# Performance work log

Hardware: AMD Instinct MI355X
Metric: run time of the kernel (lower is better)

The kernel has to match this reference:

```python
import jax, jax.numpy as jnp
import numpy as np

B_, N_, D_ = 8, 1024, 64
H_, DH_ = 4, 16
DI_, DS_, DTR_ = 128, 64, 4
MAXP = 512


def _ln(x, w, b, eps=1e-5):
    m = jnp.mean(x, -1, keepdims=True)
    v = jnp.mean((x - m) ** 2, -1, keepdims=True)
    return (x - m) * jax.lax.rsqrt(v + eps) * w + b


def _attn(x, drop_mask, Wq, Wkv, Wo, bo, rel_emb):
    b, n, d = x.shape
    scale = DH_ ** -0.5
    q = (x @ Wq).reshape(b, n, H_, DH_).transpose(0, 2, 1, 3)
    kv = x @ Wkv
    k = kv[..., :d].reshape(b, n, H_, DH_).transpose(0, 2, 1, 3)
    v = kv[..., d:].reshape(b, n, H_, DH_).transpose(0, 2, 1, 3)
    dots = jnp.einsum('bhid,bhjd->bhij', q, k) * scale
    seq = jnp.arange(n)
    dist = jnp.clip(seq[:, None] - seq[None, :], -MAXP, MAXP) + MAXP
    rpe = rel_emb[dist]  # (n, n, DH_)
    dots = dots + jnp.einsum('bhid,ijd->bhij', q, rpe) * scale
    # stochastic key drop: Bernoulli(0.3) positions get -1e12
    dots = dots + drop_mask.astype(dots.dtype) * (-1e12)
    attn = jax.nn.softmax(dots, axis=-1)
    out = jnp.einsum('bhij,bhjd->bhid', attn, v)
    out = out.transpose(0, 2, 1, 3).reshape(b, n, H_ * DH_)
    return out @ Wo + bo


def _mamba(x, W_in, conv_w, conv_b, W_xproj, W_dt, b_dt, A_log, Dm, W_out):
    b, n, _ = x.shape
    xz = x @ W_in                      # (b, n, 2*DI_)
    u, z = xz[..., :DI_], xz[..., DI_:]
    uc = u.transpose(0, 2, 1)          # (b, DI_, n)
    uc = jax.lax.conv_general_dilated(
        uc, conv_w[:, None, :], (1,), ((3, 0),),
        feature_group_count=DI_, dimension_numbers=('NCH', 'OIH', 'NCH'))
    uc = uc + conv_b[None, :, None]
    u = jax.nn.silu(uc).transpose(0, 2, 1)  # (b, n, DI_)
    xdb = u @ W_xproj                  # (b, n, DTR_+2*DS_)
    dt = jax.nn.softplus(xdb[..., :DTR_] @ W_dt + b_dt)  # (b, n, DI_)
    Bm = xdb[..., DTR_:DTR_ + DS_]
    Cm = xdb[..., DTR_ + DS_:]
    A = -jnp.exp(A_log)                # (DI_, DS_)

    def step(h, inp):
        dt_t, B_t, C_t, u_t = inp      # (b,DI_),(b,DS_),(b,DS_),(b,DI_)
        dA = jnp.exp(dt_t[..., None] * A)
        h = h * dA + (dt_t * u_t)[..., None] * B_t[:, None, :]
        y = jnp.einsum('bds,bs->bd', h, C_t)
        return h, y

    h0 = jnp.zeros((b, DI_, DS_), x.dtype)
    xs = (dt.transpose(1, 0, 2), Bm.transpose(1, 0, 2),
          Cm.transpose(1, 0, 2), u.transpose(1, 0, 2))
    _, ys = jax.lax.scan(step, h0, xs)
    y = ys.transpose(1, 0, 2) + u * Dm
    y = y * jax.nn.silu(z)
    return y @ W_out


def _rmsgn(x, gamma, eps=1e-5, groups=4):
    shp = x.shape
    dpg = shp[-1] // groups
    xg = x.reshape(shp[:-1] + (groups, dpg))
    rms = jnp.sqrt(jnp.sum(xg * xg, -1, keepdims=True)) * (dpg ** -0.5)
    return (xg / (rms + eps)).reshape(shp) * gamma


def _ff1(x, c1_w, c1_b, d1_w, d1_b):
    # SwiGLUConvDeconv1d(64, 256, kernel=4, shift=1); x: (b, s2, 64)
    s2 = x.shape[1]
    xc = x.transpose(0, 2, 1)
    xc = jnp.pad(xc, ((0, 0), (0, 0), (3, 3)))
    xc = jax.lax.conv_general_dilated(
        xc, c1_w, (1,), 'VALID', dimension_numbers=('NCH', 'OIH', 'NCH'))
    xc = xc + c1_b[None, :, None]
    gate = jax.nn.silu(xc[:, 256:, :])
    xc = xc[:, :256, :] * gate
    # ConvTranspose1d stride 1 == conv with flipped kernel, full padding
    w = jnp.flip(d1_w, -1).transpose(1, 0, 2)  # (64, 256, 4)
    xc = jax.lax.conv_general_dilated(
        xc, w, (1,), ((3, 3),), dimension_numbers=('NCH', 'OIH', 'NCH'))
    xc = xc + d1_b[None, :, None]
    out = xc.transpose(0, 2, 1)
    return out[:, 3:3 + s2, :]


def _forward(x, drop_mask, ln1_w, ln1_b, Wq, Wkv, Wo, bo, rel_emb,
             ln2_w, ln2_b, W_in, conv_w, conv_b, W_xproj, W_dt, b_dt,
             A_log, Dm, W_out, gamma, c1_w, c1_b, d1_w, d1_b, ln3_w, ln3_b):
    xt = _ln(x, ln1_w, ln1_b)
    xt = _attn(xt, drop_mask, Wq, Wkv, Wo, bo, rel_emb) + x
    x = x + xt  # dropout p=0 -> identity (faithful to original residual math)
    xt = _ln(x, ln2_w, ln2_b)
    m = _mamba(xt, W_in, conv_w, conv_b, W_xproj, W_dt, b_dt, A_log, Dm, W_out)
    m = jnp.where(m >= 0, m, 0.01 * m)  # leaky_relu
    m = _rmsgn(m, gamma)
    m = m + 0.5 * _ff1(m, c1_w, c1_b, d1_w, d1_b)
    x = x + m
    return _ln(x, ln3_w, ln3_b)


def setup_inputs() -> dict:
    ks = jax.random.split(jax.random.key(0), 16)
    g = lambda i, shp, s: jax.random.normal(ks[i], shp, dtype=jnp.float32) * s
    A_log = jnp.log(jnp.tile(jnp.arange(1, DS_ + 1, dtype=jnp.float32)[None, :], (DI_, 1)))
    return {
        'x': jax.random.normal(ks[0], (B_, N_, D_), dtype=jnp.float32),
        'drop_mask': jax.random.bernoulli(ks[1], 0.3, (B_, H_, N_, N_)),
        'ln1_w': jnp.ones((D_,), jnp.float32), 'ln1_b': jnp.zeros((D_,), jnp.float32),
        'Wq': g(2, (D_, D_), 0.1), 'Wkv': g(3, (D_, 2 * D_), 0.1),
        'Wo': g(4, (D_, D_), 0.1), 'bo': jnp.zeros((D_,), jnp.float32),
        'rel_emb': g(5, (2 * MAXP + 1, DH_), 0.02),
        'ln2_w': jnp.ones((D_,), jnp.float32), 'ln2_b': jnp.zeros((D_,), jnp.float32),
        'W_in': g(6, (D_, 2 * DI_), 0.1),
        'conv_w': g(7, (DI_, 4), 0.2), 'conv_b': jnp.zeros((DI_,), jnp.float32),
        'W_xproj': g(8, (DI_, DTR_ + 2 * DS_), 0.1),
        'W_dt': g(9, (DTR_, DI_), 0.1), 'b_dt': jnp.zeros((DI_,), jnp.float32),
        'A_log': A_log, 'Dm': jnp.ones((DI_,), jnp.float32),
        'W_out': g(10, (DI_, D_), 0.1),
        'gamma': jnp.ones((D_,), jnp.float32),
        'c1_w': g(11, (512, 64, 4), 0.1), 'c1_b': jnp.zeros((512,), jnp.float32),
        'd1_w': g(12, (256, 64, 4), 0.1), 'd1_b': jnp.zeros((64,), jnp.float32),
        'ln3_w': jnp.ones((D_,), jnp.float32), 'ln3_b': jnp.zeros((D_,), jnp.float32),
    }


def reference(x, drop_mask, ln1_w, ln1_b, Wq, Wkv, Wo, bo, rel_emb,
              ln2_w, ln2_b, W_in, conv_w, conv_b, W_xproj, W_dt, b_dt,
              A_log, Dm, W_out, gamma, c1_w, c1_b, d1_w, d1_b, ln3_w, ln3_b):
    return _forward(x, drop_mask, ln1_w, ln1_b, Wq, Wkv, Wo, bo, rel_emb,
                    ln2_w, ln2_b, W_in, conv_w, conv_b, W_xproj, W_dt, b_dt,
                    A_log, Dm, W_out, gamma, c1_w, c1_b, d1_w, d1_b, ln3_w, ln3_b)
```

## Files before the change

kernel.cpp:

```cpp
#include <hip/hip_runtime.h>
#include <math.h>


__device__ __forceinline__ float wsum64(float v){
#pragma unroll
  for(int m=32;m>0;m>>=1) v += __shfl_xor(v, m, 64);
  return v;
}
__device__ __forceinline__ float wmax64(float v){
#pragma unroll
  for(int m=32;m>0;m>>=1) v = fmaxf(v, __shfl_xor(v, m, 64));
  return v;
}
__device__ __forceinline__ float silu_f(float x){ return x / (1.f + __expf(-x)); }

__global__ __launch_bounds__(256) void k_ln1_qkv(
    const float* __restrict__ x, const float* __restrict__ w1, const float* __restrict__ b1,
    const float* __restrict__ Wq, const float* __restrict__ Wkv,
    const float* __restrict__ rel, const float* __restrict__ c1w,
    float* __restrict__ qb, float2* __restrict__ kvT,
    float* __restrict__ relT, float* __restrict__ c1wT){
  int lane = threadIdx.x & 63, warp = threadIdx.x >> 6;
  int token = blockIdx.x*4 + warp;
  __shared__ float xt[4][64];
  float xv = x[(size_t)token*64 + lane];
  float mean = wsum64(xv) * 0.015625f;
  float dlt = xv - mean;
  float var = wsum64(dlt*dlt) * 0.015625f;
  float xn = dlt * rsqrtf(var + 1e-5f) * w1[lane] + b1[lane];
  xt[warp][lane] = xn;
  __syncthreads();
  float aq=0.f, ak=0.f, av=0.f;
#pragma unroll 4
  for(int dd=0; dd<64; ++dd){
    float xd = xt[warp][dd];
    aq += xd * Wq[dd*64 + lane];
    ak += xd * Wkv[dd*128 + lane];
    av += xd * Wkv[dd*128 + 64 + lane];
  }
  int b = token >> 10, i = token & 1023;
  int h = lane >> 4, dh = lane & 15;
  size_t o  = (((size_t)(b*4 + h))*1024 + i)*16 + dh;
  size_t oT = (((size_t)(b*4 + h))*16 + dh)*1024 + i;
  qb[o]=aq;
  kvT[oT] = make_float2(ak, av);

  if (blockIdx.x < 65){
    int idx = blockIdx.x*256 + threadIdx.x;
    if (idx < 16*1025){
      int c = idx / 1025;
      int d = idx - c*1025;
      relT[idx] = rel[d*16 + c];
    }
  } else if (blockIdx.x < 577){
    int idx = (blockIdx.x-65)*256 + threadIdx.x;
    int row = idx >> 9;
    int ii  = idx & 511;
    c1wT[idx] = c1w[(size_t)ii*256 + row];
  }
}

__global__ __launch_bounds__(256) void k_kmax(
    const float2* __restrict__ kvT, float* __restrict__ Kmax){
  int bh = blockIdx.x; int tid = threadIdx.x;
  const float2* base = kvT + (size_t)bh*16*1024;
  float mx = 0.f;
#pragma unroll
  for(int r=0;r<4;++r){
    int j = tid + 256*r;
    float ss = 0.f;
#pragma unroll
    for(int c=0;c<16;++c){ float2 kv = base[c*1024 + j]; ss += kv.x*kv.x; }
    mx = fmaxf(mx, ss);
  }
  mx = wmax64(mx);
  __shared__ float red[4];
  int lane = tid&63, wv = tid>>6;
  if(lane==0) red[wv]=mx;
  __syncthreads();
  if(tid==0) Kmax[bh] = sqrtf(fmaxf(fmaxf(red[0],red[1]),fmaxf(red[2],red[3])));
}

__global__ __launch_bounds__(256, 3) void k_attn(
    const float* __restrict__ qb, const float2* __restrict__ kvT,
    const int* __restrict__ dmask, const float* __restrict__ relT,
    const float* __restrict__ Kmax, float* __restrict__ attn_raw){
  int tid = threadIdx.x;
  int lane = tid & 63, wv = tid >> 6;
  int bh  = blockIdx.y;
  int i0  = blockIdx.x*8;
  int b = bh >> 2, h = bh & 3;
  int r0 = wv*2, r1 = wv*2 + 1;

  __shared__ float Gc[8][1024];
  __shared__ float qs[8][16];
  __shared__ float G0s[8], G1024s[8];
  __shared__ float gmS[8];
  __shared__ float Ms[8];
  __shared__ float sums[8];

  if (tid < 128){
    int r = tid >> 4, c = tid & 15;
    qs[r][c] = qb[((size_t)bh*1024 + i0 + r)*16 + c] * 0.25f;
  }
  __syncthreads();

#pragma unroll 1
  for(int bb=0; bb<5; ++bb){
    int d = tid + 256*bb;
    if (d <= 1024){
      float rl[16];
#pragma unroll
      for(int c=0;c<16;++c) rl[c] = relT[c*1025 + d];
#pragma unroll
      for(int r=0;r<8;++r){
        float g = 0.f;
#pragma unroll
        for(int c=0;c<16;++c) g += qs[r][c]*rl[c];
        if (d == 0)        G0s[r] = g;
        else if (d == 1024) G1024s[r] = g;
        else {
          int j = i0 + r + 512 - d;
          if (j >= 0 && j < 1024) Gc[r][j] = g;
        }
      }
    }
  }
  __syncthreads();
#pragma unroll
  for(int r=0;r<8;++r){
    float g0 = G0s[r], g1 = G1024s[r];
    int lo = i0 + r - 512;
    int hi = i0 + r + 512;
#pragma unroll
    for(int p=0;p<4;++p){
      int j = tid + 256*p;
      if (j >= hi) Gc[r][j] = g0;
      else if (j <= lo) Gc[r][j] = g1;
    }
  }
  __syncthreads();
  {
    int r = tid >> 5, jb = tid & 31;
    float gm = -3.0e38f;
#pragma unroll
    for(int k=0;k<32;++k) gm = fmaxf(gm, Gc[r][jb + 32*k]);
#pragma unroll
    for(int m=1;m<32;m<<=1) gm = fmaxf(gm, __shfl_xor(gm, m, 64));
    if ((lane&31)==0) gmS[r] = gm;
  }
  __syncthreads();
  if (tid < 8){
    float qn = 0.f;
#pragma unroll
    for(int c=0;c<16;++c) qn += qs[tid][c]*qs[tid][c];
    Ms[tid] = gmS[tid] + sqrtf(qn)*Kmax[bh];
  }
  __syncthreads();

  float q0[16], q1[16];
#pragma unroll
  for(int c=0;c<16;++c){ q0[c]=qs[r0][c]; q1[c]=qs[r1][c]; }
  float M0 = Ms[r0], M1 = Ms[r1];

  const float2* kvb = kvT + (size_t)bh*16*1024;
  const int* mb0 = dmask + ((size_t)bh*1024 + i0 + r0)*1024;
  const int* mb1 = dmask + ((size_t)bh*1024 + i0 + r1)*1024;

  float s0=0.f, s1=0.f;
  float a0[16], a1[16];
#pragma unroll
  for(int c=0;c<16;++c){ a0[c]=0.f; a1[c]=0.f; }

#pragma unroll 1
  for(int t=0;t<16;++t){
    int j = lane + 64*t;
    int mk0 = mb0[j], mk1 = mb1[j];
    float2 kv[16];
#pragma unroll
    for(int c=0;c<16;++c) kv[c] = kvb[c*1024 + j];
    float sv0 = Gc[r0][j], sv1 = Gc[r1][j];
#pragma unroll
    for(int c=0;c<16;++c){ sv0 += q0[c]*kv[c].x; sv1 += q1[c]*kv[c].x; }
    float p0 = mk0 ? 0.f : __expf(sv0 - M0);
    float p1 = mk1 ? 0.f : __expf(sv1 - M1);
    s0 += p0; s1 += p1;
#pragma unroll
    for(int c=0;c<16;++c){ a0[c] += p0*kv[c].y; a1[c] += p1*kv[c].y; }
  }
  s0 = wsum64(s0); s1 = wsum64(s1);
#pragma unroll
  for(int c=0;c<16;++c){
    float x0 = a0[c];
    x0 += __shfl_xor(x0, 32, 64); x0 += __shfl_xor(x0, 16, 64);
    a0[c] = x0;
    float x1 = a1[c];
    x1 += __shfl_xor(x1, 32, 64); x1 += __shfl_xor(x1, 16, 64);
    a1[c] = x1;
  }
  __syncthreads();
  float* red = &Gc[0][0];
  if (lane < 16){
#pragma unroll
    for(int c=0;c<16;++c){
      red[r0*272 + lane*17 + c] = a0[c];
      red[r1*272 + lane*17 + c] = a1[c];
    }
  }
  if (lane == 0){ sums[r0] = s0; sums[r1] = s1; }
  __syncthreads();
  if (tid < 128){
    int row = tid >> 4, c = tid & 15;
    float tot = 0.f;
#pragma unroll
    for(int g=0; g<16; ++g) tot += red[row*272 + g*17 + c];
    attn_raw[((size_t)b*1024 + i0 + row)*64 + h*16 + c] = tot / sums[row];
  }
}

__global__ __launch_bounds__(256) void k_post_attn(
    const float* __restrict__ x, const float* __restrict__ attn_raw,
    const float* __restrict__ Wo, const float* __restrict__ bo,
    const float* __restrict__ ln2w, const float* __restrict__ ln2b,
    const float* __restrict__ W_in,
    float* __restrict__ x2, float* __restrict__ u0, float* __restrict__ zsarr){
  int lane = threadIdx.x & 63, warp = threadIdx.x >> 6;
  int token = blockIdx.x*4 + warp;
  __shared__ float ar[4][64];
  __shared__ float lnv[4][64];
  ar[warp][lane] = attn_raw[(size_t)token*64 + lane];
  __syncthreads();
  float acc = bo[lane];
#pragma unroll 4
  for(int dd=0;dd<64;++dd) acc += ar[warp][dd]*Wo[dd*64+lane];
  float t = 2.f*x[(size_t)token*64+lane] + acc;
  x2[(size_t)token*64+lane] = t;
  float mean = wsum64(t)*0.015625f;
  float dlt = t-mean;
  float var = wsum64(dlt*dlt)*0.015625f;
  float ln = dlt*rsqrtf(var+1e-5f)*ln2w[lane]+ln2b[lane];
  lnv[warp][lane]=ln;
  __syncthreads();
  float a0=0.f,a1=0.f,a2=0.f,a3=0.f;
#pragma unroll 4
  for(int dd=0;dd<64;++dd){
    float xd = lnv[warp][dd];
    const float* wr = W_in + dd*256;
    a0 += xd*wr[lane]; a1 += xd*wr[lane+64]; a2 += xd*wr[lane+128]; a3 += xd*wr[lane+192];
  }
  u0[(size_t)token*128 + lane] = a0;
  u0[(size_t)token*128 + 64 + lane] = a1;
  zsarr[(size_t)token*128 + lane] = silu_f(a2);
  zsarr[(size_t)token*128 + 64 + lane] = silu_f(a3);
}

__global__ __launch_bounds__(256) void k_conv_proj(
    const float* __restrict__ u0, const float* __restrict__ conv_w, const float* __restrict__ conv_b,
    const float* __restrict__ W_xproj, const float* __restrict__ W_dt, const float* __restrict__ b_dt,
    float* __restrict__ uarr, float* __restrict__ Bmp, float* __restrict__ Cmp, float* __restrict__ dtarr){
  int sub = threadIdx.x >> 7, c = threadIdx.x & 127;
  int token = blockIdx.x*2 + sub;
  int b = token >> 10, i = token & 1023;
  __shared__ float us[2][128];
  __shared__ float dtin[2][4];
  float acc = conv_b[c];
#pragma unroll
  for(int k2=0;k2<4;++k2){
    int t2 = i - 3 + k2;
    if (t2 >= 0) acc += u0[((size_t)b*1024 + t2)*128 + c]*conv_w[c*4+k2];
  }
  float uv = silu_f(acc);
  uarr[(size_t)token*128 + c] = uv;
  us[sub][c] = uv;
  __syncthreads();
  float accA = 0.f, accB = 0.f;
  int cB = 128 + (c & 3);
#pragma unroll 4
  for(int dd=0; dd<128; ++dd){
    float xd = us[sub][dd];
    accA += xd * W_xproj[dd*132 + c];
    accB += xd * W_xproj[dd*132 + cB];
  }
  if (c < 4){ dtin[sub][c] = accA; Cmp[(size_t)token*64 + 60 + c] = accB; }
  else if (c < 68) Bmp[(size_t)token*64 + (c-4)] = accA;
  else             Cmp[(size_t)token*64 + (c-68)] = accA;
  __syncthreads();
  float dv = b_dt[c];
#pragma unroll
  for(int r2=0;r2<4;++r2) dv += dtin[sub][r2]*W_dt[r2*128 + c];
  dv = fmaxf(dv, 0.f) + log1pf(expf(-fabsf(dv)));
  dtarr[(size_t)token*128 + c] = dv;
}

__global__ __launch_bounds__(256) void k_scan_a(
    const float* __restrict__ dtarr, const float* __restrict__ uarr,
    const float* __restrict__ Bmp, const float* __restrict__ A_log,
    float* __restrict__ Parr, float* __restrict__ Rarr){
  int lane = threadIdx.x & 63, warp = threadIdx.x >> 6;
  int w = blockIdx.x*4 + warp;
  int c = w & 7, d = (w >> 3) & 127, b = w >> 10;
  float A = -expf(A_log[d*64 + lane]);
  int tb = c*128;
  const float* dtp = dtarr + ((size_t)b*1024 + tb)*128 + d;
  const float* up  = uarr  + ((size_t)b*1024 + tb)*128 + d;
  const float* Bp  = Bmp   + ((size_t)b*1024 + tb)*64 + lane;
  float R = 0.f, sdt = 0.f;
  for(int t0=0; t0<128; t0+=8){
    float dtc[8], uc[8], Bc[8];
#pragma unroll
    for(int r=0;r<8;++r){
      dtc[r]=dtp[(size_t)(t0+r)*128]; uc[r]=up[(size_t)(t0+r)*128]; Bc[r]=Bp[(size_t)(t0+r)*64];
    }
#pragma unroll
    for(int r=0;r<8;++r){
      float dt = dtc[r];
      R = R*__expf(dt*A) + dt*uc[r]*Bc[r];
      sdt += dt;
    }
  }
  Parr[(size_t)w*64 + lane] = __expf(sdt*A);
  Rarr[(size_t)w*64 + lane] = R;
}

__global__ __launch_bounds__(256) void k_scan_c(
    const float* __restrict__ dtarr, const float* __restrict__ uarr,
    const float* __restrict__ Bmp, const float* __restrict__ Cmp,
    const float* __restrict__ zsarr, const float* __restrict__ A_log,
    const float* __restrict__ Dm, const float* __restrict__ Parr,
    const float* __restrict__ Rarr, float* __restrict__ ymp){
  int lane = threadIdx.x & 63, warp = threadIdx.x >> 6;
  int w = blockIdx.x*4 + warp;
  int c = w & 7, d = (w >> 3) & 127, b = w >> 10;
  float A = -expf(A_log[d*64 + lane]);
  float Dv = Dm[d];
  float h = 0.f;
  int wbase = w - c;
#pragma unroll 1
  for(int cp=0; cp<c; ++cp){
    float P = Parr[(size_t)(wbase+cp)*64 + lane];
    float R = Rarr[(size_t)(wbase+cp)*64 + lane];
    h = h*P + R;
  }
  int tb = c*128;
  const float* dtp = dtarr + ((size_t)b*1024 + tb)*128 + d;
  const float* up  = uarr  + ((size_t)b*1024 + tb)*128 + d;
  const float* zp  = zsarr + ((size_t)b*1024 + tb)*128 + d;
  const float* Bp  = Bmp   + ((size_t)b*1024 + tb)*64 + lane;
  const float* Cp  = Cmp   + ((size_t)b*1024 + tb)*64 + lane;
  float* yp        = ymp   + ((size_t)b*1024 + tb)*128 + d;
  for(int t0=0; t0<128; t0+=8){
    float dtc[8], uc[8], Bc[8], Cc[8], zc[8];
#pragma unroll
    for(int r=0;r<8;++r){
      dtc[r]=dtp[(size_t)(t0+r)*128]; uc[r]=up[(size_t)(t0+r)*128];
      Bc[r]=Bp[(size_t)(t0+r)*64];    Cc[r]=Cp[(size_t)(t0+r)*64];
      zc[r]=zp[(size_t)(t0+r)*128];
    }
    float hc[8];
#pragma unroll
    for(int r=0;r<8;++r){
      float dt = dtc[r];
      h = h*__expf(dt*A) + dt*uc[r]*Bc[r];
      hc[r] = h*Cc[r];
    }
    float y[8];
#pragma unroll
    for(int r=0;r<8;++r) y[r] = wsum64(hc[r]);
    if (lane==0){
#pragma unroll
      for(int r=0;r<8;++r) yp[(size_t)(t0+r)*128] = (y[r] + uc[r]*Dv)*zc[r];
    }
  }
}

__global__ __launch_bounds__(256) void k_wout(
    const float* __restrict__ ymp, const float* __restrict__ W_out,
    const float* __restrict__ gamma, float* __restrict__ marr){
  int lane = threadIdx.x & 63, warp = threadIdx.x >> 6;
  int token = blockIdx.x*4 + warp;
  __shared__ float ys[4][128];
  ys[warp][lane]      = ymp[(size_t)token*128 + lane];
  ys[warp][lane+64]   = ymp[(size_t)token*128 + 64 + lane];
  __syncthreads();
  float acc = 0.f;
#pragma unroll 4
  for(int dd=0; dd<128; ++dd) acc += ys[warp][dd]*W_out[dd*64 + lane];
  acc = acc >= 0.f ? acc : 0.01f*acc;
  float ss = acc*acc;
#pragma unroll
  for(int m=1;m<16;m<<=1) ss += __shfl_xor(ss, m, 64);
  float rms = sqrtf(ss)*0.25f;
  marr[(size_t)token*64 + lane] = acc/(rms + 1e-5f)*gamma[lane];
}

__global__ __launch_bounds__(256) void k_h2(
    const float* __restrict__ marr, const float* __restrict__ c1wT,
    const float* __restrict__ c1b, float* __restrict__ h2){
  int b = blockIdx.y;
  int t0 = blockIdx.x * 16;
  int tid = threadIdx.x;
  __shared__ float ms[19][64];
  for(int l = tid; l < 19*64; l += 256){
    int row = l >> 6, cc = l & 63;
    int t = t0 - 3 + row;
    ms[row][cc] = (t >= 0 && t < 1024) ? marr[((size_t)b*1024 + t)*64 + cc] : 0.f;
  }
  __syncthreads();
  int i = tid;
  float acc1[16], acc2[16];
#pragma unroll
  for(int tl=0;tl<16;++tl){ acc1[tl]=0.f; acc2[tl]=0.f; }
  for(int cc=0; cc<64; ++cc){
    float mv[19];
#pragma unroll
    for(int r2=0;r2<19;++r2) mv[r2] = ms[r2][cc];
    const float* wr = c1wT + (size_t)cc*4*512;
    float wa0 = wr[      i], wa1 = wr[ 512+i], wa2 = wr[1024+i], wa3 = wr[1536+i];
    float wg0 = wr[  256+i], wg1 = wr[ 768+i], wg2 = wr[1280+i], wg3 = wr[1792+i];
#pragma unroll
    for(int tl=0; tl<16; ++tl){
      acc1[tl] += wa0*mv[tl+0] + wa1*mv[tl+1] + wa2*mv[tl+2] + wa3*mv[tl+3];
      acc2[tl] += wg0*mv[tl+0] + wg1*mv[tl+1] + wg2*mv[tl+2] + wg3*mv[tl+3];
    }
  }
  float bb1 = c1b[i], bb2 = c1b[i+256];
#pragma unroll
  for(int tl=0; tl<16; ++tl){
    int t = t0 + tl;
    if (t < 1027){
      float o1 = acc1[tl] + bb1;
      float o2 = acc2[tl] + bb2;
      h2[((size_t)b*1027 + t)*256 + i] = o1 * silu_f(o2);
    }
  }
}

__global__ __launch_bounds__(256) void k_ff_final(
    const float* __restrict__ h2, const float* __restrict__ d1w, const float* __restrict__ d1b,
    const float* __restrict__ x2, const float* __restrict__ marr,
    const float* __restrict__ ln3w, const float* __restrict__ ln3b,
    float* __restrict__ out){
  int b = blockIdx.y;
  int s0 = blockIdx.x * 16;
  int tid = threadIdx.x;
  int o = tid & 63, sg = tid >> 6;
  __shared__ float hs[19][256];
  for(int l = tid; l < 19*256; l += 256){
    int row = l >> 8, cc = l & 255;
    hs[row][cc] = h2[((size_t)b*1027 + s0 + row)*256 + cc];
  }
  __syncthreads();
  int sl = sg*4;
  float acc0=0.f, acc1=0.f, acc2=0.f, acc3=0.f;
  const float4* wb = (const float4*)d1w + o;
#pragma unroll 2
  for(int i2=0; i2<256; ++i2){
    float4 wv = wb[(size_t)i2*64];
    float h0=hs[sl+0][i2], h1=hs[sl+1][i2], h2v=hs[sl+2][i2], h3=hs[sl+3][i2];
    float h4=hs[sl+4][i2], h5=hs[sl+5][i2], h6=hs[sl+6][i2];
    acc0 += h0*wv.w + h1*wv.z + h2v*wv.y + h3*wv.x;
    acc1 += h1*wv.w + h2v*wv.z + h3*wv.y + h4*wv.x;
    acc2 += h2v*wv.w + h3*wv.z + h4*wv.y + h5*wv.x;
    acc3 += h3*wv.w + h4*wv.z + h5*wv.y + h6*wv.x;
  }
  float accs[4] = {acc0, acc1, acc2, acc3};
  float bo_ = d1b[o];
#pragma unroll
  for(int r=0;r<4;++r){
    int s = s0 + sl + r;
    size_t idx = ((size_t)b*1024 + s)*64 + o;
    float tot = x2[idx] + marr[idx] + 0.5f*(accs[r] + bo_);
    float mean = wsum64(tot)*0.015625f;
    float dlt = tot - mean;
    float var = wsum64(dlt*dlt)*0.015625f;
    out[idx] = dlt*rsqrtf(var+1e-5f)*ln3w[o] + ln3b[o];
  }
}

extern "C" void kernel_launch(void* const* d_in, const int* in_sizes, int n_in,
                              void* d_out, int out_size, void* d_ws, size_t ws_size,
                              hipStream_t stream){
  const float* x       = (const float*)d_in[0];
  const int*   dmask   = (const int*)  d_in[1];
  const float* ln1w    = (const float*)d_in[2];
  const float* ln1b    = (const float*)d_in[3];
  const float* Wq      = (const float*)d_in[4];
  const float* Wkv     = (const float*)d_in[5];
  const float* Wo      = (const float*)d_in[6];
  const float* bo      = (const float*)d_in[7];
  const float* rel     = (const float*)d_in[8];
  const float* ln2w    = (const float*)d_in[9];
  const float* ln2b    = (const float*)d_in[10];
  const float* W_in    = (const float*)d_in[11];
  const float* conv_w  = (const float*)d_in[12];
  const float* conv_b  = (const float*)d_in[13];
  const float* W_xproj = (const float*)d_in[14];
  const float* W_dt    = (const float*)d_in[15];
  const float* b_dt    = (const float*)d_in[16];
  const float* A_log   = (const float*)d_in[17];
  const float* Dm      = (const float*)d_in[18];
  const float* W_out   = (const float*)d_in[19];
  const float* gamma   = (const float*)d_in[20];
  const float* c1w     = (const float*)d_in[21];
  const float* c1b     = (const float*)d_in[22];
  const float* d1w     = (const float*)d_in[23];
  const float* d1b     = (const float*)d_in[24];
  const float* ln3w    = (const float*)d_in[25];
  const float* ln3b    = (const float*)d_in[26];
  float* outp = (float*)d_out;

  float* ws = (float*)d_ws;
  float* qb       = ws;
  float* kvT      = qb      + 524288;
  float* attn_raw = kvT     + 1048576;
  float* x2       = attn_raw+ 524288;
  float* u0       = x2      + 524288;
  float* zsarr    = u0      + 1048576;
  float* uarr     = zsarr   + 1048576;
  float* dtarr    = uarr    + 1048576;
  float* Bmp      = dtarr   + 1048576;
  float* Cmp      = Bmp     + 524288;
  float* ymp      = Cmp     + 524288;
  float* marr     = ymp     + 1048576;
  float* h2       = marr    + 524288;
  float* relT     = h2      + 2103296;
  float* c1wT     = relT    + 16400;
  float* Parr     = c1wT    + 131072;
  float* Rarr     = Parr    + 524288;
  float* Kmaxa    = Rarr    + 524288;

  k_ln1_qkv  <<<2048, 256, 0, stream>>>(x, ln1w, ln1b, Wq, Wkv, rel, c1w,
                                        qb, (float2*)kvT, relT, c1wT);
  k_kmax     <<<32, 256, 0, stream>>>((const float2*)kvT, Kmaxa);
  k_attn     <<<dim3(128,32), 256, 0, stream>>>(qb, (const float2*)kvT, dmask, relT, Kmaxa, attn_raw);
  k_post_attn<<<2048, 256, 0, stream>>>(x, attn_raw, Wo, bo, ln2w, ln2b, W_in, x2, u0, zsarr);
  k_conv_proj<<<4096, 256, 0, stream>>>(u0, conv_w, conv_b, W_xproj, W_dt, b_dt, uarr, Bmp, Cmp, dtarr);
  k_scan_a   <<<2048, 256, 0, stream>>>(dtarr, uarr, Bmp, A_log, Parr, Rarr);
  k_scan_c   <<<2048, 256, 0, stream>>>(dtarr, uarr, Bmp, Cmp, zsarr, A_log, Dm, Parr, Rarr, ymp);
  k_wout     <<<2048, 256, 0, stream>>>(ymp, W_out, gamma, marr);
  k_h2       <<<dim3(65,8), 256, 0, stream>>>(marr, c1wT, c1b, h2);
  k_ff_final <<<dim3(64,8), 256, 0, stream>>>(h2, d1w, d1b, x2, marr, ln3w, ln3b, outp);
}
```

Measured before the change: 738.4 us.

## Tile post-attention kernel to 16 tokens per block with register-held W_in columns

k_post_attn now handles 16 tokens per block instead of 4. Each wave computes the Wo projection and LayerNorm for four tokens in sequence. Each thread then keeps one column of W_in (64 values) in registers and reuses it across all 16 tokens, reading the normalized activations from shared memory as float4. This reduces repeated global reads of W_in, at the cost of more registers per thread and a quarter as many blocks.

```diff
diff --git a/kernel.cpp b/kernel.cpp
--- a/kernel.cpp
+++ b/kernel.cpp
@@ -224,34 +224,46 @@
     const float* __restrict__ ln2w, const float* __restrict__ ln2b,
     const float* __restrict__ W_in,
     float* __restrict__ x2, float* __restrict__ u0, float* __restrict__ zsarr){
-  int lane = threadIdx.x & 63, warp = threadIdx.x >> 6;
-  int token = blockIdx.x*4 + warp;
-  __shared__ float ar[4][64];
-  __shared__ float lnv[4][64];
-  ar[warp][lane] = attn_raw[(size_t)token*64 + lane];
-  __syncthreads();
-  float acc = bo[lane];
+  int tid = threadIdx.x;
+  int lane = tid & 63, wv = tid >> 6;
+  int tok0 = blockIdx.x * 16;
+  __shared__ float arS[16][64];
+  __shared__ float lnS[16][64];
+  for(int l = tid; l < 1024; l += 256)
+    arS[l >> 6][l & 63] = attn_raw[(size_t)tok0*64 + l];
+  __syncthreads();
+#pragma unroll 1
+  for(int tt = 0; tt < 4; ++tt){
+    int tl = wv*4 + tt;
+    int token = tok0 + tl;
+    float acc = bo[lane];
 #pragma unroll 4
-  for(int dd=0;dd<64;++dd) acc += ar[warp][dd]*Wo[dd*64+lane];
-  float t = 2.f*x[(size_t)token*64+lane] + acc;
-  x2[(size_t)token*64+lane] = t;
-  float mean = wsum64(t)*0.015625f;
-  float dlt = t-mean;
-  float var = wsum64(dlt*dlt)*0.015625f;
-  float ln = dlt*rsqrtf(var+1e-5f)*ln2w[lane]+ln2b[lane];
-  lnv[warp][lane]=ln;
-  __syncthreads();
-  float a0=0.f,a1=0.f,a2=0.f,a3=0.f;
-#pragma unroll 4
-  for(int dd=0;dd<64;++dd){
-    float xd = lnv[warp][dd];
-    const float* wr = W_in + dd*256;
-    a0 += xd*wr[lane]; a1 += xd*wr[lane+64]; a2 += xd*wr[lane+128]; a3 += xd*wr[lane+192];
-  }
-  u0[(size_t)token*128 + lane] = a0;
-  u0[(size_t)token*128 + 64 + lane] = a1;
-  zsarr[(size_t)token*128 + lane] = silu_f(a2);
-  zsarr[(size_t)token*128 + 64 + lane] = silu_f(a3);
+    for(int dd = 0; dd < 64; ++dd) acc += arS[tl][dd] * Wo[dd*64 + lane];
+    float t = 2.f*x[(size_t)token*64 + lane] + acc;
+    x2[(size_t)token*64 + lane] = t;
+    float mean = wsum64(t)*0.015625f;
+    float dlt = t - mean;
+    float var = wsum64(dlt*dlt)*0.015625f;
+    lnS[tl][lane] = dlt*rsqrtf(var+1e-5f)*ln2w[lane] + ln2b[lane];
+  }
+  __syncthreads();
+  int oc = tid;
+  float w[64];
+#pragma unroll
+  for(int dd = 0; dd < 64; ++dd) w[dd] = W_in[dd*256 + oc];
+  const float4* lnS4 = (const float4*)&lnS[0][0];
+#pragma unroll 1
+  for(int tl = 0; tl < 16; ++tl){
+    float acc = 0.f;
+#pragma unroll
+    for(int d4 = 0; d4 < 16; ++d4){
+      float4 l4 = lnS4[tl*16 + d4];
+      acc += l4.x*w[4*d4] + l4.y*w[4*d4+1] + l4.z*w[4*d4+2] + l4.w*w[4*d4+3];
+    }
+    int token = tok0 + tl;
+    if (oc < 128) u0[(size_t)token*128 + oc] = acc;
+    else          zsarr[(size_t)token*128 + (oc-128)] = silu_f(acc);
+  }
 }
 
 __global__ __launch_bounds__(256) void k_conv_proj(
@@ -533,7 +545,7 @@
                                         qb, (float2*)kvT, relT, c1wT);
   k_kmax     <<<32, 256, 0, stream>>>((const float2*)kvT, Kmaxa);
   k_attn     <<<dim3(128,32), 256, 0, stream>>>(qb, (const float2*)kvT, dmask, relT, Kmaxa, attn_raw);
-  k_post_attn<<<2048, 256, 0, stream>>>(x, attn_raw, Wo, bo, ln2w, ln2b, W_in, x2, u0, zsarr);
+  k_post_attn<<<512, 256, 0, stream>>>(x, attn_raw, Wo, bo, ln2w, ln2b, W_in, x2, u0, zsarr);
   k_conv_proj<<<4096, 256, 0, stream>>>(u0, conv_w, conv_b, W_xproj, W_dt, b_dt, uarr, Bmp, Cmp, dtarr);
   k_scan_a   <<<2048, 256, 0, stream>>>(dtarr, uarr, Bmp, A_log, Parr, Rarr);
   k_scan_c   <<<2048, 256, 0, stream>>>(dtarr, uarr, Bmp, Cmp, zsarr, A_log, Dm, Parr, Rarr, ymp);
```

Measured after the change: 737.1 us. No clear change (-0.2%).
